# Performance work log

Measured on AMD Instinct MI355X. Metric: run time of the kernel, lower is better.

Reference implementation:

```python
import jax, jax.numpy as jnp
import numpy as np

B, N, K = 4, 1024, 512
HEADS, DH = 8, 64
HID = 2048
KAPPA = 1.0      # kappa_beta
ALPHA = 1e-3     # ffn_alpha (prior weight)
LAM = 1.0        # ffn_lambda_belief
NITER = 2        # ffn_n_iterations
EPS = 1e-8


def _ln(x, g, b):
    m = jnp.mean(x, axis=-1, keepdims=True)
    v = jnp.var(x, axis=-1, keepdims=True)
    return (x - m) * jax.lax.rsqrt(v + 1e-5) * g + b


def _transport(x, phi, G):
    # truncated exp(phi . G) applied to x without materializing (B,N,K,K)
    def Ax(y):
        return jnp.einsum('bng,gkl,bnl->bnk', phi, G, y)
    a1 = Ax(x)
    return x + a1 + 0.5 * Ax(a1)


def setup_inputs() -> dict:
    key = jax.random.key(0)
    ks = jax.random.split(key, 16)
    mu_q = jax.random.normal(ks[0], (B, N, K), dtype=jnp.float32)
    sigma_q = jax.random.uniform(ks[1], (B, N, K), minval=0.5, maxval=1.5, dtype=jnp.float32)
    phi = 0.1 * jax.random.normal(ks[2], (B, N, 3), dtype=jnp.float32)
    A = jax.random.normal(ks[3], (3, K, K), dtype=jnp.float32)
    generators = 0.05 * (A - jnp.transpose(A, (0, 2, 1)))  # antisymmetric Lie generators
    mask = jnp.broadcast_to(jnp.tril(jnp.ones((N, N), dtype=bool)), (B, N, N))  # causal
    mu_prior = jax.random.normal(ks[4], (B, N, K), dtype=jnp.float32)
    s = 0.02
    Wq = s * jax.random.normal(ks[5], (K, K), dtype=jnp.float32)
    Wk = s * jax.random.normal(ks[6], (K, K), dtype=jnp.float32)
    Wv = s * jax.random.normal(ks[7], (K, K), dtype=jnp.float32)
    Wo = s * jax.random.normal(ks[8], (K, K), dtype=jnp.float32)
    g1 = jnp.ones((K,), jnp.float32); be1 = jnp.zeros((K,), jnp.float32)
    g2 = jnp.ones((K,), jnp.float32); be2 = jnp.zeros((K,), jnp.float32)
    W1 = s * jax.random.normal(ks[9], (K, HID), dtype=jnp.float32)
    bh1 = jnp.zeros((HID,), jnp.float32)
    W2 = s * jax.random.normal(ks[10], (HID, K), dtype=jnp.float32)
    bh2 = jnp.zeros((K,), jnp.float32)
    lr = jnp.array(0.1, jnp.float32)  # learnable VFE step size
    return {'mu_q': mu_q, 'sigma_q': sigma_q, 'phi': phi, 'generators': generators,
            'mask': mask, 'mu_prior': mu_prior, 'Wq': Wq, 'Wk': Wk, 'Wv': Wv, 'Wo': Wo,
            'g1': g1, 'be1': be1, 'g2': g2, 'be2': be2,
            'W1': W1, 'bh1': bh1, 'W2': W2, 'bh2': bh2, 'lr': lr}


def reference(mu_q, sigma_q, phi, generators, mask, mu_prior,
              Wq, Wk, Wv, Wo, g1, be1, g2, be2, W1, bh1, W2, bh2, lr):
    # ---- attention sublayer ----
    mu_n = _ln(mu_q, g1, be1)
    mu_g = _transport(mu_n, phi, generators)  # transport to common frame

    def heads(x):  # (B,N,K) -> (B,H,N,Dh)
        return x.reshape(B, N, HEADS, DH).transpose(0, 2, 1, 3)

    q = heads(mu_g @ Wq)
    k = heads(mu_g @ Wk)
    v = heads(mu_g @ Wv)
    # diagonal covariance propagated through linear maps: var_out = sigma @ W^2
    sq = heads(sigma_q @ (Wq * Wq)) + EPS
    sk = heads(sigma_q @ (Wk * Wk)) + EPS

    inv = 1.0 / sq
    # KL(N(k_j,sk_j) || N(q_i,sq_i)) for diagonal Gaussians, decomposed into matmuls
    tr = jnp.einsum('bhid,bhjd->bhij', inv, sk)
    quad = (jnp.sum(q * q * inv, axis=-1)[..., None]
            - 2.0 * jnp.einsum('bhid,bhjd->bhij', q * inv, k)
            + jnp.einsum('bhid,bhjd->bhij', inv, k * k))
    logdet = (jnp.sum(jnp.log(sq), axis=-1)[..., None]
              - jnp.sum(jnp.log(sk), axis=-1)[:, :, None, :])
    kl = 0.5 * (tr + quad - DH + logdet)  # (B,H,N,N)

    scores = jnp.where(mask[:, None, :, :], -kl / KAPPA, -1e9)
    beta = jax.nn.softmax(scores, axis=-1)

    out = jnp.einsum('bhij,bhjd->bhid', beta, v)
    out = out.transpose(0, 2, 1, 3).reshape(B, N, K)
    mu_attn = _transport(out @ Wo, -phi, generators)  # back-transport to local frames
    mu_res = mu_q + mu_attn  # residual (dropout is identity in eval)

    # ---- VFE_dynamic FFN sublayer ----
    mu_n2 = _ln(mu_res, g2, be2)
    beta_m = jnp.mean(beta, axis=1)  # (B,N,N) attention-belief coupling
    h = mu_n2
    for _ in range(NITER):
        drive = jax.nn.gelu(h @ W1 + bh1) @ W2 + bh2
        grad = ALPHA * (h - mu_prior) + LAM * (h - jnp.einsum('bij,bjk->bik', beta_m, h))
        h = h + lr * (drive - grad)
    mu_out = mu_res + (h - mu_n2)

    return (mu_out, sigma_q, phi)
```

## Files before the change

kernel.cpp:

```cpp
#include <hip/hip_runtime.h>
#include <math.h>

#define BB 4
#define NN 1024
#define KK 512
#define HH 8
#define DHh 64
#define HIDd 2048
#define BN (BB*NN)

typedef unsigned short u16;
typedef __attribute__((ext_vector_type(8))) short bf16x8;
typedef __attribute__((ext_vector_type(4))) float f32x4;

__device__ __forceinline__ float gelu_tanh(float x){
    float u = 0.7978845608028654f*(x + 0.044715f*x*x*x);
    u = fminf(fmaxf(u, -15.f), 15.f);
    float t = __expf(2.f*u);
    return x*t/(t+1.f);
}
__device__ __forceinline__ u16 f2bf(float x){
    unsigned int u = __float_as_uint(x);
    unsigned int r = (u + 0x7fffu + ((u>>16)&1u)) >> 16;
    return (u16)r;
}
__device__ __forceinline__ float bf2f(u16 b){
    return __uint_as_float(((unsigned int)b)<<16);
}
__device__ __forceinline__ void gload16(const void* g, void* l){
    __builtin_amdgcn_global_load_lds((__attribute__((address_space(1))) void*)g,
                                     (__attribute__((address_space(3))) void*)l, 16, 0, 0);
}
__device__ __forceinline__ void wsplit(u16* hi, u16* lo, size_t o, float v){
    u16 h = f2bf(v);
    hi[o] = h;
    if (lo) lo[o] = f2bf(v - bf2f(h));
}

__global__ __launch_bounds__(256) void split_t_k(
    const float* __restrict__ src, u16* __restrict__ hi, u16* __restrict__ lo,
    int Kc, int Nc, long sS, long sD, int square)
{
    __shared__ float t[32][33];
    const int n0 = blockIdx.x*32, k0 = blockIdx.y*32, bz = blockIdx.z;
    const float* S = src + (long)bz*sS;
    const int tx = threadIdx.x & 31, ty = threadIdx.x >> 5;
    for (int r = ty; r < 32; r += 8){
        float v = S[(long)(k0+r)*Nc + n0+tx];
        if (square) v *= v;
        t[r][tx] = v;
    }
    __syncthreads();
    for (int r = ty; r < 32; r += 8){
        float v = t[tx][r];
        long o = (long)bz*sD + (long)(n0+r)*Kc + k0 + tx;
        wsplit(hi, lo, o, v);
    }
}

__global__ __launch_bounds__(256) void wmega_k(
    const float* __restrict__ Wq, const float* __restrict__ Wk,
    const float* __restrict__ Wv, const float* __restrict__ Wo,
    const float* __restrict__ W1, const float* __restrict__ W2,
    const float* __restrict__ gen,
    u16* __restrict__ WQKVh, u16* __restrict__ WQKVl, u16* __restrict__ WoTh,
    u16* __restrict__ WSQKh, u16* __restrict__ WSQKl,
    u16* __restrict__ W1Th, u16* __restrict__ W2Th, u16* __restrict__ GFh)
{
    const int z = blockIdx.z;
    const int tid = threadIdx.x;
    if (z == 8){
        if (blockIdx.x >= 48) return;
        const int c0 = blockIdx.x*32, k0 = blockIdx.y*32;
        const int tx = tid&31, ty = tid>>5;
        const int g = c0/KK, l0 = c0%KK;
        for (int r=ty; r<32; r+=8)
            GFh[(size_t)(k0+r)*(3*KK) + c0+tx] =
                f2bf(gen[(size_t)g*KK*KK + (size_t)(k0+r)*KK + l0+tx]);
        return;
    }
    __shared__ float t[32][33];
    const float* src; u16* hi; u16* lo=0; int sq=0;
    int n0, k0, Kc, Nc;
    const size_t KK2 = (size_t)KK*KK;
    if (z < 6){
        if (blockIdx.x >= 16) return;
        n0 = blockIdx.x*32; k0 = blockIdx.y*32; Kc=KK; Nc=KK;
        if      (z==0){ src=Wq; hi=WQKVh;       lo=WQKVl; }
        else if (z==1){ src=Wk; hi=WQKVh+KK2;   lo=WQKVl+KK2; }
        else if (z==2){ src=Wv; hi=WQKVh+2*KK2; lo=WQKVl+2*KK2; }
        else if (z==3){ src=Wo; hi=WoTh; }
        else if (z==4){ src=Wq; hi=WSQKh;       lo=WSQKl; sq=1; }
        else          { src=Wk; hi=WSQKh+KK2;   lo=WSQKl+KK2; sq=1; }
    } else if (z == 6){
        src=W1; hi=W1Th; Kc=KK; Nc=HIDd;
        n0 = blockIdx.x*32; k0 = blockIdx.y*32;
    } else {
        src=W2; hi=W2Th; Kc=HIDd; Nc=KK;
        n0 = blockIdx.y*32; k0 = blockIdx.x*32;
    }
    const int tx=tid&31, ty=tid>>5;
    for (int r=ty;r<32;r+=8){
        float v = src[(long)(k0+r)*Nc + n0+tx];
        if (sq) v*=v;
        t[r][tx]=v;
    }
    __syncthreads();
    for (int r=ty;r<32;r+=8){
        float v = t[tx][r];
        long o = (long)(n0+r)*Kc + k0+tx;
        wsplit(hi, lo, o, v);
    }
}

__global__ __launch_bounds__(256) void gemm_mfma_k(
    const u16* __restrict__ Ah, const u16* __restrict__ Bh,
    float* __restrict__ C, u16* __restrict__ Chi, u16* __restrict__ Clo,
    int M, int Kc, int Nc, int lda,
    long sA, long sB, long sC, const float* __restrict__ bias, int act,
    int swz,
    const u16* __restrict__ A2, const u16* __restrict__ B2,
    float* __restrict__ C2, int ycut)
{
    __shared__ u16 shA[3][128*32], shB[3][128*32];
    int bx = blockIdx.x, by = blockIdx.y;
    if (swz){
        int lin = bx + gridDim.x*by;
        int within = lin & 31, st = lin >> 5;
        int stm = gridDim.x >> 3;
        bx = (st % stm)*8 + (within & 7);
        by = (st / stm)*4 + (within >> 3);
    }
    int bz = blockIdx.z;
    int m0, n0, kend;
    const u16 *gAh, *gBh;
    if (ycut && by < ycut){
        m0 = (bx & 7)*128; n0 = by*128; bz = bx >> 3;
        gAh = A2 + (long)bz*NN*NN;
        gBh = B2 + (long)bz*KK*NN;
        Kc = NN; lda = NN; Nc = KK;
        C = C2 + (long)bz*NN*KK; Chi = 0; Clo = 0; bias = 0; act = 0; sC = 0;
        kend = m0 + 128;
        bz = 0;
    } else {
        if (ycut) by -= ycut;
        m0 = bx*128; n0 = by*128;
        gAh = Ah + (long)bz*sA;
        gBh = Bh + (long)bz*sB;
        kend = Kc;
    }
    const int tid = threadIdx.x;
    const int wave = tid >> 6, lane = tid & 63;
    const int quad = lane >> 4, r16 = lane & 15;
    const int wm = (wave>>1)*64, wn = (wave&1)*64;

    f32x4 acc[4][4];
    #pragma unroll
    for (int i=0;i<4;i++)
        #pragma unroll
        for (int j=0;j<4;j++) acc[i][j] = (f32x4){0.f,0.f,0.f,0.f};

    auto stage = [&](int sel, int k0){
        #pragma unroll
        for (int half=0; half<2; ++half){
            int c = half*256 + tid;
            int row = c >> 2;
            int kg = ((c & 3) ^ ((row >> 1) & 3))*8;
            gload16(gAh + (long)(m0+row)*lda + k0 + kg, &shA[sel][c*8]);
            gload16(gBh + (long)(n0+row)*Kc  + k0 + kg, &shB[sel][c*8]);
        }
    };

    const int nsteps = kend >> 5;
    stage(0, 0);
    if (1 < nsteps) stage(1, 1<<5);
    const int swr = (quad ^ ((r16 >> 1) & 3))*8;
    for (int t = 0; t < nsteps; ++t){
        if (t+1 < nsteps) asm volatile("s_waitcnt vmcnt(4)" ::: "memory");
        else              asm volatile("s_waitcnt vmcnt(0)" ::: "memory");
        __builtin_amdgcn_s_barrier();
        if (t+2 < nsteps) stage((t+2)%3, (t+2)<<5);
        const int rd = t % 3;
        bf16x8 afh[4], bfh[4];
        #pragma unroll
        for (int i=0;i<4;i++){
            afh[i] = *(const bf16x8*)&shA[rd][(wm+i*16+r16)*32 + swr];
            bfh[i] = *(const bf16x8*)&shB[rd][(wn+i*16+r16)*32 + swr];
        }
        #pragma unroll
        for (int i=0;i<4;i++)
            #pragma unroll
            for (int j=0;j<4;j++)
                acc[i][j] = __builtin_amdgcn_mfma_f32_16x16x32_bf16(afh[i], bfh[j], acc[i][j], 0,0,0);
    }
    #pragma unroll
    for (int i=0;i<4;i++){
        #pragma unroll
        for (int j=0;j<4;j++){
            int gc = n0 + wn + j*16 + r16;
            if (gc >= Nc) continue;
            float bv = bias ? bias[gc] : 0.f;
            #pragma unroll
            for (int r=0;r<4;r++){
                long gr = m0 + wm + i*16 + quad*4 + r;
                float v = acc[i][j][r] + bv;
                if (act) v = gelu_tanh(v);
                long o = (long)bz*sC + gr*Nc + gc;
                if (C) C[o] = v;
                if (Chi){ u16 t = f2bf(v); Chi[o] = t; if (Clo) Clo[o] = f2bf(v - bf2f(t)); }
            }
        }
    }
}

template<int NBUF>
__global__ __launch_bounds__(256) void gemm_v3_k(
    const u16* __restrict__ Ah, const u16* __restrict__ Al,
    const u16* __restrict__ Bh, const u16* __restrict__ Bl,
    float* __restrict__ C,
    int M, int Kc, int Nc, int lda,
    long sA, long sB, long sC, int cskip, int swzmode,
    const u16* __restrict__ Ah2, const u16* __restrict__ Al2,
    const u16* __restrict__ Bh2, const u16* __restrict__ Bl2,
    float* __restrict__ C2, int ycut, int Nc2,
    const float* __restrict__ dvec)
{
    __shared__ u16 shA[NBUF][128*32], shB[NBUF][128*32];
    int bx = blockIdx.x, by = blockIdx.y, bz = blockIdx.z;
    if (swzmode == 1){
        int lin = bx + gridDim.x*by;
        int within = lin & 31, st = lin >> 5;
        int stm = gridDim.x >> 3;
        bx = (st % stm)*8 + (within & 7);
        by = (st / stm)*4 + (within >> 3);
    } else if (swzmode == 2){
        int lin = bx + gridDim.x*(by + gridDim.y*bz);
        int xcd = lin & 7, idx = lin >> 3;
        bz = xcd + 8*(idx >> 6);
        int tile = idx & 63;
        bx = tile & 7; by = tile >> 3;
    }
    if (ycut && by >= ycut){
        Ah = Ah2; Al = Al2; Bh = Bh2; Bl = Bl2; C = C2;
        by -= ycut; Nc = Nc2;
    }
    const int m0 = bx*128, n0 = by*128;
    if (cskip == 1 && n0 > m0 + 127) return;
    const u16* gAh = Ah + (long)bz*sA;
    const u16* gAl = Al + (long)bz*sA;
    const u16* gBh = Bh + (long)bz*sB;
    const u16* gBl = Bl + (long)bz*sB;
    const int tid = threadIdx.x;
    const int wave = tid >> 6, lane = tid & 63;
    const int quad = lane >> 4, r16 = lane & 15;
    const int wm = (wave>>1)*64, wn = (wave&1)*64;

    f32x4 acc[4][4];
    #pragma unroll
    for (int i=0;i<4;i++)
        #pragma unroll
        for (int j=0;j<4;j++) acc[i][j] = (f32x4){0.f,0.f,0.f,0.f};

    const int segsteps = Kc >> 5;
    const int nsteps = 3*segsteps;
    auto stage = [&](int sel, int t){
        int seg = (t >= segsteps) + (t >= 2*segsteps);
        int k0 = (t - seg*segsteps) << 5;
        const u16* a = (seg==1) ? gAl : gAh;
        const u16* b = (seg==2) ? gBl : gBh;
        #pragma unroll
        for (int half=0; half<2; ++half){
            int c = half*256 + tid;
            int row = c >> 2;
            int kg = ((c & 3) ^ ((row >> 1) & 3))*8;
            gload16(a + (long)(m0+row)*lda + k0 + kg, &shA[sel][c*8]);
            gload16(b + (long)(n0+row)*Kc  + k0 + kg, &shB[sel][c*8]);
        }
    };

    const int swr = (quad ^ ((r16 >> 1) & 3))*8;
    if constexpr (NBUF == 2){
        stage(0, 0);
        __syncthreads();
        int cur = 0;
        for (int t = 0; t < nsteps; ++t){
            if (t+1 < nsteps) stage(cur^1, t+1);
            bf16x8 afh[4], bfh[4];
            #pragma unroll
            for (int i=0;i<4;i++){
                afh[i] = *(const bf16x8*)&shA[cur][(wm+i*16+r16)*32 + swr];
                bfh[i] = *(const bf16x8*)&shB[cur][(wn+i*16+r16)*32 + swr];
            }
            #pragma unroll
            for (int i=0;i<4;i++)
                #pragma unroll
                for (int j=0;j<4;j++)
                    acc[i][j] = __builtin_amdgcn_mfma_f32_16x16x32_bf16(afh[i], bfh[j], acc[i][j], 0,0,0);
            __syncthreads();
            cur ^= 1;
        }
    } else {
        stage(0, 0);
        if (1 < nsteps) stage(1, 1);
        for (int t = 0; t < nsteps; ++t){
            if (t+1 < nsteps) asm volatile("s_waitcnt vmcnt(4)" ::: "memory");
            else              asm volatile("s_waitcnt vmcnt(0)" ::: "memory");
            __builtin_amdgcn_s_barrier();
            if (t+2 < nsteps) stage((t+2)%3, t+2);
            const int rd = t % 3;
            bf16x8 afh[4], bfh[4];
            #pragma unroll
            for (int i=0;i<4;i++){
                afh[i] = *(const bf16x8*)&shA[rd][(wm+i*16+r16)*32 + swr];
                bfh[i] = *(const bf16x8*)&shB[rd][(wn+i*16+r16)*32 + swr];
            }
            #pragma unroll
            for (int i=0;i<4;i++)
                #pragma unroll
                for (int j=0;j<4;j++)
                    acc[i][j] = __builtin_amdgcn_mfma_f32_16x16x32_bf16(afh[i], bfh[j], acc[i][j], 0,0,0);
        }
    }
    float dv4[4];
    if (dvec){
        #pragma unroll
        for (int j=0;j<4;j++)
            dv4[j] = 0.5f*dvec[(size_t)bz*NN + n0 + wn + j*16 + r16];
    }
    #pragma unroll
    for (int i=0;i<4;i++){
        #pragma unroll
        for (int j=0;j<4;j++){
            int gc = n0 + wn + j*16 + r16;
            if (gc >= Nc) continue;
            #pragma unroll
            for (int r=0;r<4;r++){
                long gr = m0 + wm + i*16 + quad*4 + r;
                if (cskip == 1 && gc > gr) continue;
                long o = (long)bz*sC + gr*Nc + gc;
                float v = acc[i][j][r];
                if (dvec) v = -0.5f*v + dv4[j];
                C[o] = v;
            }
        }
    }
}

__global__ __launch_bounds__(256) void tgemm_k(
    const u16* __restrict__ Ahh,
    const u16* __restrict__ GFh,
    const float* __restrict__ phi, float esign,
    float* __restrict__ C, u16* __restrict__ Chi, u16* __restrict__ Clo,
    const float* __restrict__ t_x, const float* __restrict__ t_a1,
    const float* __restrict__ t_res)
{
    __shared__ u16 shA[3][64*64], shB[3][64*64];
    const int m0 = blockIdx.x*64, n0 = blockIdx.y*64;
    const int tid = threadIdx.x;
    const int wave = tid >> 6, lane = tid & 63;
    const int quad = lane >> 4, r16 = lane & 15;
    const int wr = wave*16;

    float ph[3][4];
    #pragma unroll
    for (int sgi=0; sgi<3; ++sgi)
        #pragma unroll
        for (int r=0; r<4; ++r)
            ph[sgi][r] = esign*phi[(size_t)(m0+wr+quad*4+r)*3 + sgi];

    f32x4 acc[4], tot[4];
    #pragma unroll
    for (int j=0;j<4;j++){ acc[j] = (f32x4){0.f,0.f,0.f,0.f}; tot[j] = acc[j]; }

    auto stage = [&](int sel, int t){
        int seg = t >> 3, k0 = (t & 7) << 6;
        #pragma unroll
        for (int rep=0; rep<2; ++rep){
            int c = rep*256 + tid;
            int row = c >> 3;
            int kg = ((c & 7) ^ (row & 7))*8;
            gload16(Ahh + (long)(m0+row)*KK + k0 + kg, &shA[sel][c*8]);
            gload16(GFh + (long)(n0+row)*(3*KK) + seg*KK + k0 + kg, &shB[sel][c*8]);
        }
    };

    stage(0, 0);
    stage(1, 1);
    for (int t = 0; t < 24; ++t){
        if (t+1 < 24) asm volatile("s_waitcnt vmcnt(4)" ::: "memory");
        else          asm volatile("s_waitcnt vmcnt(0)" ::: "memory");
        __builtin_amdgcn_s_barrier();
        if (t+2 < 24) stage((t+2)%3, t+2);
        const int rd = t % 3;
        #pragma unroll
        for (int kk=0; kk<2; ++kk){
            const int s = (((kk<<2)+quad) ^ (r16 & 7))*8;
            bf16x8 af = *(const bf16x8*)&shA[rd][(wr+r16)*64 + s];
            #pragma unroll
            for (int j=0;j<4;j++){
                bf16x8 bh = *(const bf16x8*)&shB[rd][(j*16+r16)*64 + s];
                acc[j] = __builtin_amdgcn_mfma_f32_16x16x32_bf16(af, bh, acc[j], 0,0,0);
            }
        }
        if ((t & 7) == 7){
            int sgi = t >> 3;
            #pragma unroll
            for (int j=0;j<4;j++){
                #pragma unroll
                for (int r=0;r<4;r++) tot[j][r] += ph[sgi][r]*acc[j][r];
                acc[j] = (f32x4){0.f,0.f,0.f,0.f};
            }
        }
    }
    #pragma unroll
    for (int j=0;j<4;j++){
        int gc = n0 + j*16 + r16;
        #pragma unroll
        for (int r=0;r<4;r++){
            long gr = m0 + wr + quad*4 + r;
            float v = tot[j][r];
            long o = gr*(long)KK + gc;
            if (t_x){
                v = t_x[o] + t_a1[o] + 0.5f*v;
                if (t_res) v += t_res[o];
            }
            if (C) C[o] = v;
            if (Chi){ u16 t2 = f2bf(v); Chi[o] = t2; if (Clo) Clo[o] = f2bf(v - bf2f(t2)); }
        }
    }
}

__global__ __launch_bounds__(256) void gemm64_k(
    const u16* __restrict__ Ah, const u16* __restrict__ Bh,
    float* __restrict__ C, u16* __restrict__ Chi, u16* __restrict__ Clo,
    int M, int Kc, int Nc, int lda,
    long sA, long sB, long sC, const float* __restrict__ bias, int act,
    int ktrim, int swz,
    const float* __restrict__ f_hin, const float* __restrict__ f_bmh,
    const float* __restrict__ f_mup, const float* __restrict__ f_lr,
    u16* __restrict__ f_hh, float* __restrict__ f_hout,
    const float* __restrict__ f_mrb, const float* __restrict__ f_mn2,
    float* __restrict__ f_out, int fmode)
{
    __shared__ u16 shA[3][64*64], shB[3][64*64];
    int bx = blockIdx.x, by = blockIdx.y;
    if (swz){
        int lin = bx + gridDim.x*by;
        int within = lin & 31, st = lin >> 5;
        int stm = gridDim.x >> 3;
        bx = (st % stm)*8 + (within & 7);
        by = (st / stm)*4 + (within >> 3);
    }
    const int m0 = bx*64, n0 = by*64;
    const int bz = blockIdx.z;
    const u16* gA = Ah + (long)bz*sA;
    const u16* gB = Bh + (long)bz*sB;
    const int tid = threadIdx.x;
    const int wave = tid >> 6, lane = tid & 63;
    const int quad = lane >> 4, r16 = lane & 15;
    const int wr = wave*16;
    const int kend = ktrim ? min(Kc, m0 + 64) : Kc;
    const int nsteps = kend >> 6;

    f32x4 acc[4];
    #pragma unroll
    for (int j=0;j<4;j++) acc[j] = (f32x4){0.f,0.f,0.f,0.f};

    auto stage = [&](int sel, int k0){
        #pragma unroll
        for (int rep=0; rep<2; ++rep){
            int c = rep*256 + tid;
            int row = c >> 3;
            int kg = ((c & 7) ^ (row & 7))*8;
            gload16(gA + (long)(m0+row)*lda + k0 + kg, &shA[sel][c*8]);
            gload16(gB + (long)(n0+row)*Kc + k0 + kg, &shB[sel][c*8]);
        }
    };

    stage(0, 0);
    if (1 < nsteps) stage(1, 1<<6);
    for (int t = 0; t < nsteps; ++t){
        if (t+1 < nsteps) asm volatile("s_waitcnt vmcnt(4)" ::: "memory");
        else              asm volatile("s_waitcnt vmcnt(0)" ::: "memory");
        __builtin_amdgcn_s_barrier();
        if (t+2 < nsteps) stage((t+2)%3, (t+2)<<6);
        const int rd = t % 3;
        #pragma unroll
        for (int kk=0; kk<2; ++kk){
            const int s = (((kk<<2)+quad) ^ (r16 & 7))*8;
            bf16x8 af = *(const bf16x8*)&shA[rd][(wr+r16)*64 + s];
            #pragma unroll
            for (int j=0;j<4;j++){
                bf16x8 bh = *(const bf16x8*)&shB[rd][(j*16+r16)*64 + s];
                acc[j] = __builtin_amdgcn_mfma_f32_16x16x32_bf16(af, bh, acc[j], 0,0,0);
            }
        }
    }
    float lrv = 0.f;
    if (fmode) lrv = *f_lr;
    #pragma unroll
    for (int j=0;j<4;j++){
        int gc = n0 + j*16 + r16;
        float bv = bias ? bias[gc] : 0.f;
        #pragma unroll
        for (int r=0;r<4;r++){
            long gr = m0 + wr + quad*4 + r;
            float v = acc[j][r] + bv;
            if (act) v = gelu_tanh(v);
            long o = (long)bz*sC + gr*Nc + gc;
            if (fmode){
                float hv = f_hin[o];
                float val = hv + lrv*(v - (1e-3f*(hv - f_mup[o]) + (hv - f_bmh[o])));
                if (fmode == 1){ f_hout[o] = val; f_hh[o] = f2bf(val); }
                else           { f_out[o] = f_mrb[o] + val - f_mn2[o]; }
            } else {
                if (C) C[o] = v;
                if (Chi){ u16 t = f2bf(v); Chi[o] = t; if (Clo) Clo[o] = f2bf(v - bf2f(t)); }
            }
        }
    }
}

__global__ __launch_bounds__(256) void ln_k(
    const float* __restrict__ x, const float* __restrict__ g,
    const float* __restrict__ be, float* __restrict__ y,
    u16* __restrict__ yh16,
    const float* __restrict__ sg, u16* __restrict__ sgh, u16* __restrict__ sgl,
    float* __restrict__ osig, const float* __restrict__ phi, float* __restrict__ ophi)
{
    __shared__ float sh[8];
    const int r = blockIdx.x, tid = threadIdx.x;
    const float* xr = x + (long)r*KK;
    float2 v = *(const float2*)(xr + tid*2);
    float s = v.x+v.y, s2 = v.x*v.x+v.y*v.y;
    #pragma unroll
    for (int o=32;o>0;o>>=1){ s += __shfl_down(s,o); s2 += __shfl_down(s2,o); }
    if ((tid&63)==0){ sh[tid>>6]=s; sh[4+(tid>>6)]=s2; }
    __syncthreads();
    s  = sh[0]+sh[1]+sh[2]+sh[3];
    s2 = sh[4]+sh[5]+sh[6]+sh[7];
    const float mean = s*(1.f/KK);
    const float var  = s2*(1.f/KK) - mean*mean;
    const float rs = rsqrtf(var + 1e-5f);
    float2 gg = *(const float2*)(g + tid*2);
    float2 bb = *(const float2*)(be + tid*2);
    float ox = (v.x-mean)*rs*gg.x + bb.x;
    float oy = (v.y-mean)*rs*gg.y + bb.y;
    long o = (long)r*KK + tid*2;
    *(float2*)(y + o) = make_float2(ox, oy);
    if (yh16){ yh16[o] = f2bf(ox); yh16[o+1] = f2bf(oy); }
    if (sgh){
        float2 sv = *(const float2*)(sg + o);
        wsplit(sgh, sgl, o,   sv.x);
        wsplit(sgh, sgl, o+1, sv.y);
        if (osig) *(float2*)(osig + o) = sv;
    }
    if (ophi && tid < 3) ophi[(size_t)r*3 + tid] = phi[(size_t)r*3 + tid];
}

__global__ __launch_bounds__(512) void prepvt_k(
    const float* __restrict__ QKV, const float* __restrict__ SQSK,
    u16* __restrict__ CFh, u16* __restrict__ CFl,
    u16* __restrict__ KSh, u16* __restrict__ KSl, float* __restrict__ dvec,
    u16* __restrict__ VTh)
{
    __shared__ float t[64][65];
    const int bx = blockIdx.x;
    const int tid = threadIdx.x;
    if (bx < BN){
        const int bn = bx;
        const int b = bn / NN, n = bn % NN;
        const int h = tid >> 6, d = tid & 63;
        float q  = QKV[(size_t)bn*1536 + h*DHh + d];
        float k  = QKV[(size_t)bn*1536 + KK + h*DHh + d];
        float sq = SQSK[(size_t)bn*1024 + h*DHh + d] + 1e-8f;
        float sk = SQSK[(size_t)bn*1024 + KK + h*DHh + d] + 1e-8f;
        float inv = 1.f/sq;
        float nqi = -2.f*q*inv;
        float skk = sk + k*k;
        const size_t base = ((size_t)(h*BB + b)*NN + n)*128;
        wsplit(CFh, CFl, base+d,    inv);
        wsplit(CFh, CFl, base+64+d, nqi);
        wsplit(KSh, KSl, base+d,    skk);
        wsplit(KSh, KSl, base+64+d, k);
        float dv = __logf(sk);
        #pragma unroll
        for (int o=32;o>0;o>>=1) dv += __shfl_down(dv,o);
        if (d==0) dvec[((size_t)h*BB + b)*NN + n] = dv;
        return;
    }
    const int idx = bx - BN;
    const int n0 = (idx & 15)*64;
    const int h = (idx>>4)&7;
    const int b = idx>>7;
    const int c4 = (tid & 15) * 4;
    const int r0 = tid >> 4;
    for (int rr = r0; rr < 64; rr += 32){
        float4 v = *(const float4*)(QKV + (size_t)(b*NN + n0 + rr)*1536 + 1024 + h*DHh + c4);
        t[c4+0][rr] = v.x; t[c4+1][rr] = v.y; t[c4+2][rr] = v.z; t[c4+3][rr] = v.w;
    }
    __syncthreads();
    for (int dd = r0; dd < 64; dd += 32){
        size_t base = ((size_t)(h*BB + b)*64 + dd)*NN + n0 + c4;
        #pragma unroll
        for (int q=0;q<4;q++) VTh[base+q] = f2bf(t[dd][c4+q]);
    }
}

__global__ __launch_bounds__(256) void softmax_all_k(
    float* __restrict__ S, u16* __restrict__ BMh)
{
    __shared__ float s_redA[2][4], s_redB[2][4];
    const int tid = threadIdx.x;
    const int b = blockIdx.x >> 10, i = blockIdx.x & (NN-1);
    const int L = i + 1;
    const int JEND = ((i >> 6) + 1) << 6;
    const int JEND2 = ((i >> 7) + 1) << 7;
    const int j4 = tid*4;
    const bool act = (j4 < JEND);
    const int wv = tid >> 6;
    const bool lane0 = ((tid & 63) == 0);

    float bm[4] = {0.f,0.f,0.f,0.f};
    float4 rv = make_float4(0,0,0,0);
    if (act) rv = *(const float4*)(S + ((long)(0*BB + b)*NN + i)*NN + j4);
    for (int h = 0; h < 8; ++h){
        const int z = h*BB + b;
        float4 rvn = make_float4(0,0,0,0);
        if (h < 7 && act){
            const int zn = (h+1)*BB + b;
            rvn = *(const float4*)(S + ((long)zn*NN + i)*NN + j4);
        }
        float sc[4];
        const float* rp = (const float*)&rv;
        #pragma unroll
        for (int e=0;e<4;e++)
            sc[e] = (act && (j4 + e < L)) ? rp[e] : -3.0e38f;
        float lm = fmaxf(fmaxf(sc[0],sc[1]), fmaxf(sc[2],sc[3]));
        #pragma unroll
        for (int o=32;o>0;o>>=1) lm = fmaxf(lm, __shfl_xor(lm, o));
        if (lane0) s_redA[h&1][wv] = lm;
        __syncthreads();
        const float mx = fmaxf(fmaxf(s_redA[h&1][0],s_redA[h&1][1]),
                               fmaxf(s_redA[h&1][2],s_redA[h&1][3]));
        float w4[4], ps = 0.f;
        #pragma unroll
        for (int e=0;e<4;e++){
            float e1 = (act && (j4 + e < L)) ? __expf(sc[e]-mx) : 0.f;
            w4[e] = e1; ps += e1;
        }
        #pragma unroll
        for (int o=32;o>0;o>>=1) ps += __shfl_xor(ps, o);
        if (lane0) s_redB[h&1][wv] = ps;
        __syncthreads();
        const float isum = 1.f/(s_redB[h&1][0]+s_redB[h&1][1]+s_redB[h&1][2]+s_redB[h&1][3]);
        if (act){
            u16* brow = (u16*)(S + ((long)z*NN + i)*NN);
            ushort4 st;
            float w0=w4[0]*isum, w1=w4[1]*isum, w2=w4[2]*isum, w3=w4[3]*isum;
            bm[0]+=0.125f*w0; bm[1]+=0.125f*w1; bm[2]+=0.125f*w2; bm[3]+=0.125f*w3;
            st.x=f2bf(w0); st.y=f2bf(w1); st.z=f2bf(w2); st.w=f2bf(w3);
            *(ushort4*)(brow + j4) = st;
        }
        rv = rvn;
    }
    if (j4 < JEND2){
        const long bmrow = ((long)b*NN + i)*NN;
        ushort4 st;
        st.x=f2bf(bm[0]); st.y=f2bf(bm[1]); st.z=f2bf(bm[2]); st.w=f2bf(bm[3]);
        *(ushort4*)(BMh + bmrow + j4) = st;
    }
}

__global__ __launch_bounds__(256) void pv_k(
    const u16* __restrict__ Sbeta,
    const u16* __restrict__ VTh,
    u16* __restrict__ xh)
{
    __shared__ u16 shA[2][64*64], shB[2][64*64];
    const int m0 = blockIdx.x*64;
    const int z = blockIdx.y;
    const int b = z & 3, head = z >> 2;
    const int tid = threadIdx.x;
    const int wave = tid>>6, lane = tid&63;
    const int quad = lane>>4, r16 = lane&15;
    f32x4 acc[4];
    #pragma unroll
    for (int j=0;j<4;j++) acc[j]=(f32x4){0.f,0.f,0.f,0.f};
    const int nsteps = (m0 >> 6) + 1;

    auto stage = [&](int sel, int j0){
        #pragma unroll
        for (int rep=0; rep<2; ++rep){
            int c = rep*256 + tid;
            int row = c >> 3;
            int k8 = ((c & 7) ^ (row & 7))*8;
            gload16(Sbeta + ((size_t)(z*NN + m0 + row))*(2*NN) + j0 + k8, &shA[sel][c*8]);
            gload16(VTh + ((size_t)(z*64 + row))*NN + j0 + k8, &shB[sel][c*8]);
        }
    };

    stage(0, 0);
    __syncthreads();
    int cur = 0;
    for (int t = 0; t < nsteps; ++t){
        if (t+1 < nsteps) stage(cur^1, (t+1)<<6);
        #pragma unroll
        for (int kk=0; kk<2; ++kk){
            const int s = (((kk<<2)+quad) ^ (r16 & 7))*8;
            bf16x8 af = *(const bf16x8*)&shA[cur][(wave*16 + r16)*64 + s];
            #pragma unroll
            for (int nj=0; nj<4; ++nj){
                bf16x8 bh = *(const bf16x8*)&shB[cur][(nj*16 + r16)*64 + s];
                acc[nj] = __builtin_amdgcn_mfma_f32_16x16x32_bf16(af, bh, acc[nj], 0,0,0);
            }
        }
        __syncthreads();
        cur ^= 1;
    }
    #pragma unroll
    for (int nj=0;nj<4;nj++){
        #pragma unroll
        for (int r=0;r<4;r++){
            int i = m0 + wave*16 + quad*4 + r;
            int d = nj*16 + r16;
            size_t o = ((size_t)(b*NN)+i)*KK + head*64 + d;
            xh[o] = f2bf(acc[nj][r]);
        }
    }
}

extern "C" void kernel_launch(void* const* d_in, const int* in_sizes, int n_in,
                              void* d_out, int out_size, void* d_ws, size_t ws_size,
                              hipStream_t stream) {
    const float* mu_q    = (const float*)d_in[0];
    const float* sigma_q = (const float*)d_in[1];
    const float* phi     = (const float*)d_in[2];
    const float* gen     = (const float*)d_in[3];
    const float* mu_prior= (const float*)d_in[5];
    const float* Wq = (const float*)d_in[6];
    const float* Wk = (const float*)d_in[7];
    const float* Wv = (const float*)d_in[8];
    const float* Wo = (const float*)d_in[9];
    const float* g1 = (const float*)d_in[10];
    const float* be1= (const float*)d_in[11];
    const float* g2 = (const float*)d_in[12];
    const float* be2= (const float*)d_in[13];
    const float* W1 = (const float*)d_in[14];
    const float* bh1= (const float*)d_in[15];
    const float* W2 = (const float*)d_in[16];
    const float* bh2= (const float*)d_in[17];
    const float* lr = (const float*)d_in[18];
    float* out = (float*)d_out;

    float* w = (float*)d_ws;
    size_t off = 0;
    auto alloc = [&](size_t n){ float* p = w + off; off += (n+3)&~(size_t)3; return p; };
    auto ualloc = [&](size_t n){ return (u16*)alloc((n+1)/2); };

    float* Xb   = alloc((size_t)BN*KK);
    float* A1b  = alloc((size_t)BN*KK);
    float* A2b  = alloc((size_t)BN*KK);
    float* QKVb = alloc((size_t)BN*3*KK);
    float* SQSKb= alloc((size_t)BN*2*KK);
    float* REG  = alloc((size_t)16*NN*NN);
    float* Sbig = Xb;
    u16*  SGh   = (u16*)REG;
    u16*  SGl   = SGh + (size_t)BN*KK;
    u16*  Xh    = SGl + (size_t)BN*KK;
    u16*  A1h   = Xh  + (size_t)BN*KK;
    u16*  WOh   = A1h + (size_t)BN*KK;
    u16*  ZH    = (u16*)REG;
    float* Db_  = alloc((size_t)HH*BB*NN);
    u16* AH  = ualloc((size_t)BN*HIDd); u16* AL  = ualloc((size_t)BN*HIDd);
    u16* CFh = AH;
    u16* CFl = AH + (size_t)HH*BB*NN*128;
    u16* KSh = AL;
    u16* KSl = AL + (size_t)HH*BB*NN*128;
    u16* VTh = ualloc((size_t)HH*BB*64*NN);
    u16* GFh = ualloc((size_t)3*KK*KK);
    u16* WQKVh= ualloc((size_t)3*KK*KK); u16* WQKVl= ualloc((size_t)3*KK*KK);
    u16* WSQKh= ualloc((size_t)2*KK*KK); u16* WSQKl= ualloc((size_t)2*KK*KK);
    u16* WoTh= ualloc((size_t)KK*KK);
    u16* W1Th= ualloc((size_t)KK*HIDd);
    u16* W2Th= ualloc((size_t)KK*HIDd);
    u16* BMh = ualloc((size_t)BB*NN*NN);
    u16* HTh = ualloc((size_t)BB*KK*NN);
    float* WOb = QKVb;
    float* Hb  = QKVb + (size_t)BN*KK;
    float* MRb = QKVb + 2*(size_t)BN*KK;
    float* MN2b= Xb;
    (void)A2b;

    {
        dim3 gw(64, 16, 9);
        wmega_k<<<gw, 256, 0, stream>>>(Wq, Wk, Wv, Wo, W1, W2, gen,
                                        WQKVh, WQKVl, WoTh, WSQKh, WSQKl,
                                        W1Th, W2Th, GFh);
    }

    ln_k<<<BN, 256, 0, stream>>>(mu_q, g1, be1, Xb, Xh, sigma_q, SGh, SGl,
                                 out + (size_t)BN*KK, phi, out + 2*(size_t)BN*KK);
    {
        dim3 tg(BN/64, KK/64, 1);
        tgemm_k<<<tg, 256, 0, stream>>>(Xh, GFh, phi, 1.f, A1b, A1h, 0, 0, 0, 0);
        tgemm_k<<<tg, 256, 0, stream>>>(A1h, GFh, phi, 1.f, 0, AH, AL, Xb, A1b, 0);
    }

    {
        dim3 g(BN/128, 20, 1);
        gemm_v3_k<3><<<g, 256, 0, stream>>>(AH, AL, WQKVh, WQKVl, QKVb,
            BN, KK, 3*KK, KK, 0, 0, 0, 0, 1,
            SGh, SGl, WSQKh, WSQKl, SQSKb, 12, 2*KK, 0);
    }
    prepvt_k<<<BN + 512, 512, 0, stream>>>(QKVb, SQSKb, CFh, CFl, KSh, KSl, Db_, VTh);

    {
        dim3 sg(NN/128, NN/128, 32);
        gemm_v3_k<2><<<sg, 256, 0, stream>>>(CFh, CFl, KSh, KSl, Sbig,
            NN, 128, NN, 128, (long)NN*128, (long)NN*128, (long)NN*NN, 1, 2,
            0, 0, 0, 0, 0, 0, 0, Db_);
        softmax_all_k<<<BB*NN, 256, 0, stream>>>(Sbig, BMh);
        dim3 pg(NN/64, 32, 1);
        pv_k<<<pg, 256, 0, stream>>>((const u16*)Sbig, VTh, AH);
    }

    {
        dim3 wg(BN/64, KK/64, 1);
        gemm64_k<<<wg, 256, 0, stream>>>(AH, WoTh, WOb, WOh, 0,
            BN, KK, KK, KK, 0,0,0, nullptr, 0, 0, 0,
            0,0,0,0,0,0,0,0,0,0);
        dim3 tg(BN/64, KK/64, 1);
        tgemm_k<<<tg, 256, 0, stream>>>(WOh, GFh, phi, -1.f, A1b, A1h, 0, 0, 0, 0);
        tgemm_k<<<tg, 256, 0, stream>>>(A1h, GFh, phi, -1.f, MRb, 0, 0, WOb, A1b, mu_q);
    }
    ln_k<<<BN, 256, 0, stream>>>(MRb, g2, be2, MN2b, AH, 0, 0, 0, 0, 0, 0);

    for (int it=0; it<2; ++it){
        const float* hin = (it==0) ? MN2b : Hb;
        {
            dim3 tg(KK/32, NN/32, BB);
            split_t_k<<<tg, 256, 0, stream>>>(hin, HTh, 0, NN, KK,
                                              (long)NN*KK, (long)KK*NN, 0);
        }
        {
            dim3 wg1(BN/128, 4 + HIDd/128, 1);
            gemm_mfma_k<<<wg1, 256, 0, stream>>>(AH, W1Th, 0, ZH, 0,
                BN, KK, HIDd, KK, 0, 0, 0, bh1, 1, 1,
                BMh, HTh, A1b, 4);
        }
        {
            dim3 wg(BN/64, KK/64, 1);
            gemm64_k<<<wg, 256, 0, stream>>>(ZH, W2Th, 0,0,0,
                                             BN, HIDd, KK, HIDd, 0,0,0, bh2, 0, 0, 1,
                                             hin, A1b, mu_prior, lr, AH, Hb, MRb, MN2b, out,
                                             (it==0) ? 1 : 2);
        }
    }

    (void)in_sizes; (void)n_in; (void)out_size; (void)ws_size;
}
```

Before: 523.9 us.

## Batch softmax reductions across heads and triple-buffer PV loads

After: 538.1 us, median of 2. 1.03x slower.

```diff
diff --git a/kernel.cpp b/kernel.cpp
--- a/kernel.cpp
+++ b/kernel.cpp
@@ -610,7 +610,7 @@
 __global__ __launch_bounds__(256) void softmax_all_k(
     float* __restrict__ S, u16* __restrict__ BMh)
 {
-    __shared__ float s_redA[2][4], s_redB[2][4];
+    __shared__ float s_redA[4][8], s_redB[4][8];
     const int tid = threadIdx.x;
     const int b = blockIdx.x >> 10, i = blockIdx.x & (NN-1);
     const int L = i + 1;
@@ -621,48 +621,66 @@
     const int wv = tid >> 6;
     const bool lane0 = ((tid & 63) == 0);
 
+    float4 rv[8];
+    #pragma unroll
+    for (int h=0; h<8; ++h){
+        rv[h] = make_float4(0,0,0,0);
+        if (act) rv[h] = *(const float4*)(S + ((long)(h*BB + b)*NN + i)*NN + j4);
+    }
+    float lm[8];
+    #pragma unroll
+    for (int h=0; h<8; ++h){
+        float* rp = (float*)&rv[h];
+        #pragma unroll
+        for (int e=0;e<4;e++)
+            rp[e] = (act && (j4 + e < L)) ? rp[e] : -3.0e38f;
+        lm[h] = fmaxf(fmaxf(rp[0],rp[1]), fmaxf(rp[2],rp[3]));
+    }
+    #pragma unroll
+    for (int h=0; h<8; ++h)
+        #pragma unroll
+        for (int o=32;o>0;o>>=1) lm[h] = fmaxf(lm[h], __shfl_xor(lm[h], o));
+    if (lane0){
+        #pragma unroll
+        for (int h=0; h<8; ++h) s_redA[wv][h] = lm[h];
+    }
+    __syncthreads();
+    float ps[8];
+    #pragma unroll
+    for (int h=0; h<8; ++h){
+        const float mx = fmaxf(fmaxf(s_redA[0][h],s_redA[1][h]),
+                               fmaxf(s_redA[2][h],s_redA[3][h]));
+        float* rp = (float*)&rv[h];
+        float p = 0.f;
+        #pragma unroll
+        for (int e=0;e<4;e++){
+            float e1 = (act && (j4 + e < L)) ? __expf(rp[e]-mx) : 0.f;
+            rp[e] = e1; p += e1;
+        }
+        ps[h] = p;
+    }
+    #pragma unroll
+    for (int h=0; h<8; ++h)
+        #pragma unroll
+        for (int o=32;o>0;o>>=1) ps[h] += __shfl_xor(ps[h], o);
+    if (lane0){
+        #pragma unroll
+        for (int h=0; h<8; ++h) s_redB[wv][h] = ps[h];
+    }
+    __syncthreads();
     float bm[4] = {0.f,0.f,0.f,0.f};
-    float4 rv = make_float4(0,0,0,0);
-    if (act) rv = *(const float4*)(S + ((long)(0*BB + b)*NN + i)*NN + j4);
-    for (int h = 0; h < 8; ++h){
-        const int z = h*BB + b;
-        float4 rvn = make_float4(0,0,0,0);
-        if (h < 7 && act){
-            const int zn = (h+1)*BB + b;
-            rvn = *(const float4*)(S + ((long)zn*NN + i)*NN + j4);
-        }
-        float sc[4];
-        const float* rp = (const float*)&rv;
-        #pragma unroll
-        for (int e=0;e<4;e++)
-            sc[e] = (act && (j4 + e < L)) ? rp[e] : -3.0e38f;
-        float lm = fmaxf(fmaxf(sc[0],sc[1]), fmaxf(sc[2],sc[3]));
-        #pragma unroll
-        for (int o=32;o>0;o>>=1) lm = fmaxf(lm, __shfl_xor(lm, o));
-        if (lane0) s_redA[h&1][wv] = lm;
-        __syncthreads();
-        const float mx = fmaxf(fmaxf(s_redA[h&1][0],s_redA[h&1][1]),
-                               fmaxf(s_redA[h&1][2],s_redA[h&1][3]));
-        float w4[4], ps = 0.f;
-        #pragma unroll
-        for (int e=0;e<4;e++){
-            float e1 = (act && (j4 + e < L)) ? __expf(sc[e]-mx) : 0.f;
-            w4[e] = e1; ps += e1;
-        }
-        #pragma unroll
-        for (int o=32;o>0;o>>=1) ps += __shfl_xor(ps, o);
-        if (lane0) s_redB[h&1][wv] = ps;
-        __syncthreads();
-        const float isum = 1.f/(s_redB[h&1][0]+s_redB[h&1][1]+s_redB[h&1][2]+s_redB[h&1][3]);
+    #pragma unroll
+    for (int h=0; h<8; ++h){
+        const float isum = 1.f/(s_redB[0][h]+s_redB[1][h]+s_redB[2][h]+s_redB[3][h]);
         if (act){
-            u16* brow = (u16*)(S + ((long)z*NN + i)*NN);
+            const float* rp = (const float*)&rv[h];
+            u16* brow = (u16*)(S + ((long)(h*BB + b)*NN + i)*NN);
             ushort4 st;
-            float w0=w4[0]*isum, w1=w4[1]*isum, w2=w4[2]*isum, w3=w4[3]*isum;
+            float w0=rp[0]*isum, w1=rp[1]*isum, w2=rp[2]*isum, w3=rp[3]*isum;
             bm[0]+=0.125f*w0; bm[1]+=0.125f*w1; bm[2]+=0.125f*w2; bm[3]+=0.125f*w3;
             st.x=f2bf(w0); st.y=f2bf(w1); st.z=f2bf(w2); st.w=f2bf(w3);
             *(ushort4*)(brow + j4) = st;
         }
-        rv = rvn;
     }
     if (j4 < JEND2){
         const long bmrow = ((long)b*NN + i)*NN;
@@ -677,7 +695,7 @@
     const u16* __restrict__ VTh,
     u16* __restrict__ xh)
 {
-    __shared__ u16 shA[2][64*64], shB[2][64*64];
+    __shared__ u16 shA[3][64*64], shB[3][64*64];
     const int m0 = blockIdx.x*64;
     const int z = blockIdx.y;
     const int b = z & 3, head = z >> 2;
@@ -701,22 +719,23 @@
     };
 
     stage(0, 0);
-    __syncthreads();
-    int cur = 0;
+    if (1 < nsteps) stage(1, 1<<6);
     for (int t = 0; t < nsteps; ++t){
-        if (t+1 < nsteps) stage(cur^1, (t+1)<<6);
+        if (t+1 < nsteps) asm volatile("s_waitcnt vmcnt(4)" ::: "memory");
+        else              asm volatile("s_waitcnt vmcnt(0)" ::: "memory");
+        __builtin_amdgcn_s_barrier();
+        if (t+2 < nsteps) stage((t+2)%3, (t+2)<<6);
+        const int rd = t % 3;
         #pragma unroll
         for (int kk=0; kk<2; ++kk){
             const int s = (((kk<<2)+quad) ^ (r16 & 7))*8;
-            bf16x8 af = *(const bf16x8*)&shA[cur][(wave*16 + r16)*64 + s];
+            bf16x8 af = *(const bf16x8*)&shA[rd][(wave*16 + r16)*64 + s];
             #pragma unroll
             for (int nj=0; nj<4; ++nj){
-                bf16x8 bh = *(const bf16x8*)&shB[cur][(nj*16 + r16)*64 + s];
+                bf16x8 bh = *(const bf16x8*)&shB[rd][(nj*16 + r16)*64 + s];
                 acc[nj] = __builtin_amdgcn_mfma_f32_16x16x32_bf16(af, bh, acc[nj], 0,0,0);
             }
         }
-        __syncthreads();
-        cur ^= 1;
     }
     #pragma unroll
     for (int nj=0;nj<4;nj++){
```
